# Performance work log

Hardware: AMD Instinct MI355X
Metric: run time of the kernel (lower is better)

## Reference

```python
import jax, jax.numpy as jnp
import numpy as np

B, A, NC, DIR, LMAX, MAXZ, NORB = 8, 64, 128, 4, 2, 10, 14
NF = NC * DIR * (2 * LMAX + 1)   # 2560
O2 = NORB * NORB                 # 196
AO = A * NORB                    # 896
LOG2 = float(np.log(2.0))

def ssp(v):  # spk shifted softplus
    return jax.nn.softplus(v) - LOG2

def setup_inputs():
    key = jax.random.key(0)
    ks = jax.random.split(key, 12)
    Z = jax.random.randint(ks[0], (B, A), 1, MAXZ)
    idx = np.arange(A)
    nbh_np = np.stack([np.delete(idx, i) for i in range(A)], 0)  # [A, A-1]: all atoms except self
    nbh = jnp.asarray(np.broadcast_to(nbh_np[None], (B, A, A - 1)).copy(), dtype=jnp.int32)
    x = jax.random.normal(ks[1], (B, A, NC), jnp.float32)
    Vijkl = jax.random.normal(ks[2], (B, A, A - 1, NF), jnp.float32) * 0.1
    sc = 1.0 / np.sqrt(NF)
    W_off = jax.random.normal(ks[3], (NF, O2), jnp.float32) * sc
    b_off = jnp.zeros((O2,), jnp.float32)
    W_on = jax.random.normal(ks[4], (NF, O2), jnp.float32) * sc
    b_on = jnp.zeros((O2,), jnp.float32)
    W_ovoff = jax.random.normal(ks[5], (NF, O2), jnp.float32) * sc
    b_ovoff = jnp.zeros((O2,), jnp.float32)
    ov_emb = jax.random.normal(ks[6], (MAXZ, O2), jnp.float32) * 0.1  # trainable overlap onsite embedding
    orb_energies = jax.random.normal(ks[7], (MAXZ, NORB), jnp.float32)  # h0 energies
    s0_energies = jnp.ones((MAXZ, NORB), jnp.float32)                   # s0 init = ones
    W1 = jax.random.normal(ks[8], (NC, NC // 2), jnp.float32) / np.sqrt(NC)
    b1 = jnp.zeros((NC // 2,), jnp.float32)
    W2 = jax.random.normal(ks[9], (NC // 2, 1), jnp.float32) / np.sqrt(NC // 2)
    b2 = jnp.zeros((1,), jnp.float32)
    return {"Z": Z, "nbh": nbh, "x": x, "Vijkl": Vijkl,
            "W_off": W_off, "b_off": b_off, "W_on": W_on, "b_on": b_on,
            "W_ovoff": W_ovoff, "b_ovoff": b_ovoff, "ov_emb": ov_emb,
            "orb_energies": orb_energies, "s0_energies": s0_energies,
            "W1": W1, "b1": b1, "W2": W2, "b2": b2}

def reference(Z, nbh, x, Vijkl, W_off, b_off, W_on, b_on, W_ovoff, b_ovoff,
              ov_emb, orb_energies, s0_energies, W1, b1, W2, b2):
    # permutation that reorders neighbor slots (plus appended zero/self slot) into atom order
    ar = jnp.broadcast_to(jnp.arange(A, dtype=nbh.dtype)[None, :, None], (B, A, 1))
    sort_idx = jnp.argsort(jnp.concatenate([nbh, ar], axis=2), axis=2)  # [B,A,A]
    eyeA = jnp.eye(A, dtype=Vijkl.dtype)
    eyeAO = jnp.eye(AO, dtype=Vijkl.dtype)

    def assemble(off, on):
        # off: [B,A,A-1,O2] pair blocks; on: [B,A,O2] onsite blocks
        offz = jnp.concatenate([off, jnp.zeros((B, A, 1, O2), off.dtype)], axis=2)  # zero self block at slot A-1
        offg = jnp.take_along_axis(offz, sort_idx[..., None], axis=2)               # [B,A,A,O2]
        M = offg + eyeA[None, :, :, None] * on[:, :, None, :]
        M = M.reshape(B, A, A, NORB, NORB).transpose(0, 1, 3, 2, 4).reshape(B, AO, AO)
        return 0.5 * (M + M.transpose(0, 2, 1))

    # Hamiltonian: offsite Dense + onsite Dense mean-aggregated over pairs
    H_off = Vijkl @ W_off + b_off                       # [B,A,A-1,O2]
    H_on = jnp.mean(Vijkl @ W_on + b_on, axis=2)        # [B,A,O2]
    H = assemble(H_off, H_on)
    # h0 single-atom diagonal (orb mask is all-active -> full diagonal)
    H = H + eyeAO[None] * orb_energies[Z].reshape(B, 1, AO)

    # Overlap: offsite Dense + onsite embedding lookup
    S_off = Vijkl @ W_ovoff + b_ovoff
    S_on = ov_emb[Z]                                    # [B,A,O2]
    S = assemble(S_off, S_on)
    S = S + eyeAO[None] * s0_energies[Z].reshape(B, 1, AO)

    # energy head: Dense->ssp->Dense->ScaleShift(0,1), sum over atoms
    Ei = ssp(x @ W1 + b1) @ W2 + b2                     # [B,A,1]
    E = jnp.sum(Ei, axis=1)                             # [B,1]
    return H, S, E
```

## Files before the change

kernel.cpp:

```cpp
#include <hip/hip_runtime.h>

#define B_      8
#define A_      64
#define NPAIR   63
#define NC_     128
#define NF_     2560
#define O2_     196
#define NORB_   14
#define AO_     896
#define NCOLS   588
#define CSTRIDE 640
#define KSTEPS  80
#define BM      128
#define BN      640

typedef short bf16x8 __attribute__((ext_vector_type(8)));
typedef float f32x4  __attribute__((ext_vector_type(4)));

__device__ __forceinline__ unsigned f2bf(float f) {
    unsigned u = __builtin_bit_cast(unsigned, f);
    return (u + 0x7fffu + ((u >> 16) & 1u)) >> 16;
}

__global__ void prep_w(const float* __restrict__ W_off, const float* __restrict__ W_ovoff,
                       const float* __restrict__ W_on, unsigned short* __restrict__ Bws) {
    __shared__ float wt[32 * BN];
    const int ks = blockIdx.x, t = threadIdx.x;
    for (int e = t; e < 32 * BN; e += 256) {
        int kl = e / BN, c = e - kl * BN;
        int kg = ks * 32 + kl;
        float v = 0.f;
        if (c < O2_)          v = W_off  [(size_t)kg * O2_ + c];
        else if (c < 2 * O2_) v = W_ovoff[(size_t)kg * O2_ + (c - O2_)];
        else if (c < 3 * O2_) v = W_on   [(size_t)kg * O2_ + (c - 2 * O2_)];
        wt[kl * BN + c] = v;
    }
    __syncthreads();
    char* out = (char*)(Bws + (size_t)ks * (BN * 32));
    for (int e = t; e < BN * 4; e += 256) {
        int n = e >> 2, sg = e & 3;
        uint4 w;
        w.x = f2bf(wt[(sg * 8 + 0) * BN + n]) | (f2bf(wt[(sg * 8 + 1) * BN + n]) << 16);
        w.y = f2bf(wt[(sg * 8 + 2) * BN + n]) | (f2bf(wt[(sg * 8 + 3) * BN + n]) << 16);
        w.z = f2bf(wt[(sg * 8 + 4) * BN + n]) | (f2bf(wt[(sg * 8 + 5) * BN + n]) << 16);
        w.w = f2bf(wt[(sg * 8 + 6) * BN + n]) | (f2bf(wt[(sg * 8 + 7) * BN + n]) << 16);
        unsigned byte = ((unsigned)(n * 64 + sg * 16)) ^ ((unsigned)(n & 7) << 4);
        *(uint4*)(out + byte) = w;
    }
}

__global__ __launch_bounds__(1024, 4)
void gemm_off(const float* __restrict__ V, const unsigned short* __restrict__ Bws,
              const float* __restrict__ b_off, const float* __restrict__ b_ovoff,
              const float* __restrict__ b_on, float* __restrict__ HSoff) {
    __shared__ alignas(16) unsigned short Alds[2][BM * 32];
    __shared__ alignas(16) unsigned short Blds[2][BN * 32];

    const int tid  = threadIdx.x;
    const int mt   = blockIdx.x;
    const int lane = tid & 63;
    const int wv   = tid >> 6;
    const int wm   = wv >> 2, wn = wv & 3;
    const int wvu  = __builtin_amdgcn_readfirstlane(wv);

    const int arow = tid >> 3, aseg = tid & 7;
    const float* aptr = V + (size_t)(mt * BM + arow) * NF_ + aseg * 4;

    f32x4 acc[2][10];
#pragma unroll
    for (int mf = 0; mf < 2; ++mf)
#pragma unroll
        for (int nf = 0; nf < 10; ++nf)
            acc[mf][nf] = (f32x4){0.f, 0.f, 0.f, 0.f};

    float4 pv;

    auto issueB = [&](int bf, int ks) {
        const unsigned short* src0 = Bws + (size_t)ks * (BN * 32) + lane * 8;
        unsigned short* dst0 = &Blds[bf][0];
        {
            __builtin_amdgcn_global_load_lds(
                (const __attribute__((address_space(1))) void*)(src0 + wvu * 512),
                (__attribute__((address_space(3))) void*)(dst0 + wvu * 512), 16, 0, 0);
        }
        {
            __builtin_amdgcn_global_load_lds(
                (const __attribute__((address_space(1))) void*)(src0 + (wvu + 16) * 512),
                (__attribute__((address_space(3))) void*)(dst0 + (wvu + 16) * 512), 16, 0, 0);
        }
        if (wvu < 8) {
            __builtin_amdgcn_global_load_lds(
                (const __attribute__((address_space(1))) void*)(src0 + (wvu + 32) * 512),
                (__attribute__((address_space(3))) void*)(dst0 + (wvu + 32) * 512), 16, 0, 0);
        }
    };
    auto loadA = [&](int ks) {
        pv = *(const float4*)(aptr + ks * 32);
    };
    auto writeA = [&](int bf) {
        uint2 w;
        w.x = f2bf(pv.x) | (f2bf(pv.y) << 16);
        w.y = f2bf(pv.z) | (f2bf(pv.w) << 16);
        unsigned byte = ((unsigned)(arow * 64 + aseg * 8)) ^ ((unsigned)(arow & 7) << 4);
        *(uint2*)((char*)&Alds[bf][0] + byte) = w;
    };
    auto compute = [&](int bf) {
        const int r0 = wm * 32 + (lane & 15);
        const int r1 = r0 + 16;
        const unsigned kb = (unsigned)(lane >> 4) * 16;
        const unsigned ab0 = ((unsigned)(r0 * 64) + kb) ^ ((unsigned)(r0 & 7) << 4);
        const unsigned ab1 = ((unsigned)(r1 * 64) + kb) ^ ((unsigned)(r1 & 7) << 4);
        bf16x8 af0 = *(const bf16x8*)((const char*)&Alds[bf][0] + ab0);
        bf16x8 af1 = *(const bf16x8*)((const char*)&Alds[bf][0] + ab1);
        const int nbase = wn * 160 + (lane & 15);
        const char* Bb = (const char*)&Blds[bf][0];
        bf16x8 bfr[2];
        {
            const int n0 = nbase;
            const unsigned b0 = ((unsigned)(n0 * 64) + kb) ^ ((unsigned)(n0 & 7) << 4);
            bfr[0] = *(const bf16x8*)(Bb + b0);
        }
#pragma unroll
        for (int nf = 0; nf < 10; ++nf) {
            if (nf < 9) {
                const int nn = nbase + (nf + 1) * 16;
                const unsigned bb = ((unsigned)(nn * 64) + kb) ^ ((unsigned)(nn & 7) << 4);
                bfr[(nf + 1) & 1] = *(const bf16x8*)(Bb + bb);
            }
            acc[0][nf] = __builtin_amdgcn_mfma_f32_16x16x32_bf16(af0, bfr[nf & 1], acc[0][nf], 0, 0, 0);
            acc[1][nf] = __builtin_amdgcn_mfma_f32_16x16x32_bf16(af1, bfr[nf & 1], acc[1][nf], 0, 0, 0);
        }
    };

    issueB(0, 0); loadA(0); writeA(0);
    __syncthreads();

    for (int ks = 0; ks < KSTEPS; ++ks) {
        const int cur = ks & 1, nxt = cur ^ 1;
        if (ks + 1 < KSTEPS) { issueB(nxt, ks + 1); loadA(ks + 1); }
        compute(cur);
        if (ks + 1 < KSTEPS) writeA(nxt);
        __syncthreads();
    }

    const int c16 = lane & 15, rg = lane >> 4;
#pragma unroll
    for (int nf = 0; nf < 10; ++nf) {
        int C = wn * 160 + nf * 16 + c16;
        if (C >= NCOLS) continue;
        float bias = (C < O2_) ? b_off[C] : (C < 2 * O2_) ? b_ovoff[C - O2_] : b_on[C - 2 * O2_];
#pragma unroll
        for (int mf = 0; mf < 2; ++mf) {
            int R = mt * BM + wm * 32 + mf * 16 + rg * 4;
            float* o = HSoff + (size_t)R * CSTRIDE + C;
            o[0]           = acc[mf][nf][0] + bias;
            o[CSTRIDE]     = acc[mf][nf][1] + bias;
            o[2 * CSTRIDE] = acc[mf][nf][2] + bias;
            o[3 * CSTRIDE] = acc[mf][nf][3] + bias;
        }
    }
}

__global__ void hon_reduce(const float* __restrict__ HSoff, float* __restrict__ Hon) {
    const int g = blockIdx.x;
    const int t = threadIdx.x;
    if (t >= O2_) return;
    const float* p0 = HSoff + (size_t)g * NPAIR * CSTRIDE + 2 * O2_ + t;
    const float* p1 = p0 + (size_t)21 * CSTRIDE;
    const float* p2 = p0 + (size_t)42 * CSTRIDE;
    float a0 = 0.f, a1 = 0.f, a2 = 0.f;
#pragma unroll 3
    for (int j = 0; j < 21; ++j) {
        a0 += p0[0]; a1 += p1[0]; a2 += p2[0];
        p0 += CSTRIDE; p1 += CSTRIDE; p2 += CSTRIDE;
    }
    Hon[(size_t)g * O2_ + t] = (a0 + a1 + a2) * (1.f / (float)NPAIR);
}

__global__ __launch_bounds__(256)
void assemble_k(const float* __restrict__ HSoff, const float* __restrict__ Hon,
                const int* __restrict__ Z, const float* __restrict__ ov_emb,
                const float* __restrict__ orbE, const float* __restrict__ s0E,
                float* __restrict__ H, float* __restrict__ S) {
    __shared__ float Ai[NPAIR * 197];
    __shared__ float Bj[2][16 * 200];
    __shared__ float Dg[O2_];
    __shared__ float Dd[NORB_];

    const int bid = blockIdx.x;
    const int h = bid & 1, i = (bid >> 1) & 63, b = bid >> 7;
    const int t = threadIdx.x;
    const int g = b * A_ + i;
    const int z = Z[g];
    float* out = (h ? S : H) + (size_t)b * AO_ * AO_;

    const float* abase = HSoff + (size_t)g * NPAIR * CSTRIDE + h * O2_;
    for (int u = t; u < NPAIR * O2_; u += 256) {
        int jj = u / O2_, e = u - jj * O2_;
        Ai[jj * 197 + e] = abase[(size_t)jj * CSTRIDE + e];
    }
    if (t < O2_)   Dg[t] = h ? ov_emb[(size_t)z * O2_ + t]   : Hon[(size_t)g * O2_ + t];
    if (t < NORB_) Dd[t] = h ? s0E[(size_t)z * NORB_ + t]    : orbE[(size_t)z * NORB_ + t];

    auto stageB = [&](int buf, int jc) {
        for (int u = t; u < 16 * O2_; u += 256) {
            int jl = u / O2_, e = u - jl * O2_;
            int j = jc * 16 + jl;
            if (j != i) {
                int idx = (i < j) ? i : i - 1;
                Bj[buf][jl * 200 + e] =
                    HSoff[((size_t)(b * A_ + j) * NPAIR + idx) * CSTRIDE + h * O2_ + e];
            }
        }
    };
    stageB(0, 0);
    __syncthreads();

    const int tj = t / NORB_, tq = t - tj * NORB_;
    for (int jc = 0; jc < 4; ++jc) {
        if (jc < 3) stageB((jc + 1) & 1, jc + 1);
        if (t < 224) {
            const int j = jc * 16 + tj;
            const int cur = jc & 1;
#pragma unroll
            for (int p = 0; p < NORB_; ++p) {
                float v;
                if (j == i) {
                    v = 0.5f * (Dg[p * NORB_ + tq] + Dg[tq * NORB_ + p]);
                    if (p == tq) v += Dd[p];
                } else {
                    int jj = (j < i) ? j : j - 1;
                    v = 0.5f * (Ai[jj * 197 + p * NORB_ + tq] + Bj[cur][tj * 200 + tq * NORB_ + p]);
                }
                out[(size_t)(i * NORB_ + p) * AO_ + jc * 224 + t] = v;
            }
        }
        __syncthreads();
    }
}

__global__ void energy_k(const float* __restrict__ x, const float* __restrict__ W1,
                         const float* __restrict__ b1, const float* __restrict__ W2,
                         const float* __restrict__ b2, float* __restrict__ E) {
    __shared__ float partial[8];
    const int b = blockIdx.x;
    const int lane = threadIdx.x & 63;
    const int w = threadIdx.x >> 6;
    float esum = 0.f;
    for (int aa = 0; aa < 8; ++aa) {
        const int a = w * 8 + aa;
        const float* xr = x + (size_t)(b * A_ + a) * NC_;
        float hj = b1[lane];
        for (int k = 0; k < NC_; ++k) hj = fmaf(xr[k], W1[k * 64 + lane], hj);
        float sp = fmaxf(hj, 0.f) + log1pf(expf(-fabsf(hj))) - 0.69314718055994531f;
        float v = sp * W2[lane];
        for (int off = 32; off; off >>= 1) v += __shfl_down(v, off);
        if (lane == 0) esum += v + b2[0];
    }
    if (lane == 0) partial[w] = esum;
    __syncthreads();
    if (threadIdx.x == 0) {
        float e = 0.f;
        for (int k = 0; k < 8; ++k) e += partial[k];
        E[b] = e;
    }
}

extern "C" void kernel_launch(void* const* d_in, const int* in_sizes, int n_in,
                              void* d_out, int out_size, void* d_ws, size_t ws_size,
                              hipStream_t stream) {
    const int*   Z       = (const int*)  d_in[0];
    const float* x       = (const float*)d_in[2];
    const float* V       = (const float*)d_in[3];
    const float* W_off   = (const float*)d_in[4];
    const float* b_off   = (const float*)d_in[5];
    const float* W_on    = (const float*)d_in[6];
    const float* b_on    = (const float*)d_in[7];
    const float* W_ovoff = (const float*)d_in[8];
    const float* b_ovoff = (const float*)d_in[9];
    const float* ov_emb  = (const float*)d_in[10];
    const float* orbE    = (const float*)d_in[11];
    const float* s0E     = (const float*)d_in[12];
    const float* W1      = (const float*)d_in[13];
    const float* b1      = (const float*)d_in[14];
    const float* W2      = (const float*)d_in[15];
    const float* b2      = (const float*)d_in[16];

    float* H = (float*)d_out;
    float* S = H + (size_t)B_ * AO_ * AO_;
    float* E = S + (size_t)B_ * AO_ * AO_;

    char* ws = (char*)d_ws;
    unsigned short* Bws = (unsigned short*)ws;
    float* HSoff = (float*)(ws + (size_t)4  * 1024 * 1024);
    float* Hon   = (float*)(ws + (size_t)88 * 1024 * 1024);

    prep_w    <<<KSTEPS, 256,  0, stream>>>(W_off, W_ovoff, W_on, Bws);
    gemm_off  <<<252,    1024, 0, stream>>>(V, Bws, b_off, b_ovoff, b_on, HSoff);
    hon_reduce<<<512,    256,  0, stream>>>(HSoff, Hon);
    assemble_k<<<1024,   256,  0, stream>>>(HSoff, Hon, Z, ov_emb, orbE, s0E, H, S);
    energy_k  <<<8,      512,  0, stream>>>(x, W1, b1, W2, b2, E);
}
```

Measured before the change: 308.8 us.

## Load B fragments directly from global into registers, drop B LDS staging

The GEMM no longer stages the bf16 weight tile through LDS. Each wave reads its B fragments straight from global/L2 into registers, with a software prefetch of the next k-step. Blocks shrink to 512 threads and each wave handles 64 rows (4 M fragments), so every B fragment feeds four MFMAs, and the A tile is written with 16-byte stores. The aim is to cut LDS traffic and barrier cost, at the price of many more global loads of B and much higher register pressure, which can limit occupancy.

Measured after the change: 307.5 us. No clear change (-0.4%).

```diff
diff --git a/kernel.cpp b/kernel.cpp
--- a/kernel.cpp
+++ b/kernel.cpp
@@ -13,6 +13,7 @@
 #define KSTEPS  80
 #define BM      128
 #define BN      640
+#define BSTEP_BYTES 40960
 
 typedef short bf16x8 __attribute__((ext_vector_type(8)));
 typedef float f32x4  __attribute__((ext_vector_type(4)));
@@ -36,7 +37,7 @@
         wt[kl * BN + c] = v;
     }
     __syncthreads();
-    char* out = (char*)(Bws + (size_t)ks * (BN * 32));
+    unsigned short* out = Bws + (size_t)ks * (BN * 32);
     for (int e = t; e < BN * 4; e += 256) {
         int n = e >> 2, sg = e & 3;
         uint4 w;
@@ -44,103 +45,97 @@
         w.y = f2bf(wt[(sg * 8 + 2) * BN + n]) | (f2bf(wt[(sg * 8 + 3) * BN + n]) << 16);
         w.z = f2bf(wt[(sg * 8 + 4) * BN + n]) | (f2bf(wt[(sg * 8 + 5) * BN + n]) << 16);
         w.w = f2bf(wt[(sg * 8 + 6) * BN + n]) | (f2bf(wt[(sg * 8 + 7) * BN + n]) << 16);
-        unsigned byte = ((unsigned)(n * 64 + sg * 16)) ^ ((unsigned)(n & 7) << 4);
-        *(uint4*)(out + byte) = w;
-    }
-}
-
-__global__ __launch_bounds__(1024, 4)
+        *(uint4*)(out + (size_t)n * 32 + sg * 8) = w;
+    }
+}
+
+__global__ __launch_bounds__(512, 2)
 void gemm_off(const float* __restrict__ V, const unsigned short* __restrict__ Bws,
               const float* __restrict__ b_off, const float* __restrict__ b_ovoff,
               const float* __restrict__ b_on, float* __restrict__ HSoff) {
     __shared__ alignas(16) unsigned short Alds[2][BM * 32];
-    __shared__ alignas(16) unsigned short Blds[2][BN * 32];
 
     const int tid  = threadIdx.x;
     const int mt   = blockIdx.x;
     const int lane = tid & 63;
     const int wv   = tid >> 6;
     const int wm   = wv >> 2, wn = wv & 3;
-    const int wvu  = __builtin_amdgcn_readfirstlane(wv);
-
-    const int arow = tid >> 3, aseg = tid & 7;
-    const float* aptr = V + (size_t)(mt * BM + arow) * NF_ + aseg * 4;
-
-    f32x4 acc[2][10];
-#pragma unroll
-    for (int mf = 0; mf < 2; ++mf)
+
+    const int arow = tid >> 2, aseg = tid & 3;
+    const float* aptr = V + (size_t)(mt * BM + arow) * NF_ + aseg * 8;
+
+    const char* bp = (const char*)Bws + (size_t)(wn * 160 + (lane & 15)) * 64 + (lane >> 4) * 16;
+#define BFRAG(t_, nf_) (*(const bf16x8*)(bp + (size_t)(t_) * BSTEP_BYTES + (nf_) * 1024))
+
+    f32x4 acc[4][10];
+#pragma unroll
+    for (int mf = 0; mf < 4; ++mf)
 #pragma unroll
         for (int nf = 0; nf < 10; ++nf)
             acc[mf][nf] = (f32x4){0.f, 0.f, 0.f, 0.f};
 
-    float4 pv;
-
-    auto issueB = [&](int bf, int ks) {
-        const unsigned short* src0 = Bws + (size_t)ks * (BN * 32) + lane * 8;
-        unsigned short* dst0 = &Blds[bf][0];
-        {
-            __builtin_amdgcn_global_load_lds(
-                (const __attribute__((address_space(1))) void*)(src0 + wvu * 512),
-                (__attribute__((address_space(3))) void*)(dst0 + wvu * 512), 16, 0, 0);
-        }
-        {
-            __builtin_amdgcn_global_load_lds(
-                (const __attribute__((address_space(1))) void*)(src0 + (wvu + 16) * 512),
-                (__attribute__((address_space(3))) void*)(dst0 + (wvu + 16) * 512), 16, 0, 0);
-        }
-        if (wvu < 8) {
-            __builtin_amdgcn_global_load_lds(
-                (const __attribute__((address_space(1))) void*)(src0 + (wvu + 32) * 512),
-                (__attribute__((address_space(3))) void*)(dst0 + (wvu + 32) * 512), 16, 0, 0);
-        }
-    };
+    float4 pv0, pv1;
     auto loadA = [&](int ks) {
-        pv = *(const float4*)(aptr + ks * 32);
+        const float* s = aptr + ks * 32;
+        pv0 = ((const float4*)s)[0];
+        pv1 = ((const float4*)s)[1];
     };
     auto writeA = [&](int bf) {
-        uint2 w;
-        w.x = f2bf(pv.x) | (f2bf(pv.y) << 16);
-        w.y = f2bf(pv.z) | (f2bf(pv.w) << 16);
-        unsigned byte = ((unsigned)(arow * 64 + aseg * 8)) ^ ((unsigned)(arow & 7) << 4);
-        *(uint2*)((char*)&Alds[bf][0] + byte) = w;
+        uint4 w;
+        w.x = f2bf(pv0.x) | (f2bf(pv0.y) << 16);
+        w.y = f2bf(pv0.z) | (f2bf(pv0.w) << 16);
+        w.z = f2bf(pv1.x) | (f2bf(pv1.y) << 16);
+        w.w = f2bf(pv1.z) | (f2bf(pv1.w) << 16);
+        unsigned byte = ((unsigned)(arow * 64 + aseg * 16)) ^ ((unsigned)(arow & 7) << 4);
+        *(uint4*)((char*)&Alds[bf][0] + byte) = w;
     };
-    auto compute = [&](int bf) {
-        const int r0 = wm * 32 + (lane & 15);
-        const int r1 = r0 + 16;
-        const unsigned kb = (unsigned)(lane >> 4) * 16;
-        const unsigned ab0 = ((unsigned)(r0 * 64) + kb) ^ ((unsigned)(r0 & 7) << 4);
-        const unsigned ab1 = ((unsigned)(r1 * 64) + kb) ^ ((unsigned)(r1 & 7) << 4);
-        bf16x8 af0 = *(const bf16x8*)((const char*)&Alds[bf][0] + ab0);
-        bf16x8 af1 = *(const bf16x8*)((const char*)&Alds[bf][0] + ab1);
-        const int nbase = wn * 160 + (lane & 15);
-        const char* Bb = (const char*)&Blds[bf][0];
-        bf16x8 bfr[2];
-        {
-            const int n0 = nbase;
-            const unsigned b0 = ((unsigned)(n0 * 64) + kb) ^ ((unsigned)(n0 & 7) << 4);
-            bfr[0] = *(const bf16x8*)(Bb + b0);
+
+    const int ar = wm * 64 + (lane & 15);
+    const unsigned kb = (unsigned)(lane >> 4) * 16;
+
+#define ARD(mf_) (*(const bf16x8*)((const char*)Ab + ((((unsigned)((ar + (mf_) * 16) * 64) + kb)) ^ ((unsigned)(ar & 7) << 4))))
+
+#define MFMA4(bv_, nf_) {                                                                  \
+    acc[0][nf_] = __builtin_amdgcn_mfma_f32_16x16x32_bf16(af0, bv_, acc[0][nf_], 0, 0, 0); \
+    acc[1][nf_] = __builtin_amdgcn_mfma_f32_16x16x32_bf16(af1, bv_, acc[1][nf_], 0, 0, 0); \
+    acc[2][nf_] = __builtin_amdgcn_mfma_f32_16x16x32_bf16(af2, bv_, acc[2][nf_], 0, 0, 0); \
+    acc[3][nf_] = __builtin_amdgcn_mfma_f32_16x16x32_bf16(af3, bv_, acc[3][nf_], 0, 0, 0); }
+
+    bf16x8 bq0, bq1, bq2, bq3, bq4;
+
+    loadA(0);
+    writeA(0);
+    bq0 = BFRAG(0, 0); bq1 = BFRAG(0, 1); bq2 = BFRAG(0, 2); bq3 = BFRAG(0, 3); bq4 = BFRAG(0, 4);
+    loadA(1);
+    asm volatile("s_waitcnt lgkmcnt(0)" ::: "memory");
+    __builtin_amdgcn_s_barrier();
+    __builtin_amdgcn_sched_barrier(0);
+
+    int cur = 0;
+    for (int t = 0; t < KSTEPS; ++t) {
+        const unsigned short* Ab = &Alds[cur][0];
+        bf16x8 af0 = ARD(0), af1 = ARD(1), af2 = ARD(2), af3 = ARD(3);
+
+        MFMA4(bq0, 0); bq0 = BFRAG(t, 5);
+        MFMA4(bq1, 1); bq1 = BFRAG(t, 6);
+        MFMA4(bq2, 2); bq2 = BFRAG(t, 7);
+        MFMA4(bq3, 3); bq3 = BFRAG(t, 8);
+        MFMA4(bq4, 4); bq4 = BFRAG(t, 9);
+        MFMA4(bq0, 5); bq0 = BFRAG(t + 1, 0);
+        MFMA4(bq1, 6); bq1 = BFRAG(t + 1, 1);
+        MFMA4(bq2, 7); bq2 = BFRAG(t + 1, 2);
+        MFMA4(bq3, 8); bq3 = BFRAG(t + 1, 3);
+        MFMA4(bq4, 9); bq4 = BFRAG(t + 1, 4);
+
+        if (t < KSTEPS - 1) {
+            writeA(cur ^ 1);
+            int ks2 = t + 2 < KSTEPS ? t + 2 : KSTEPS - 1;
+            loadA(ks2);
+            asm volatile("s_waitcnt lgkmcnt(0)" ::: "memory");
+            __builtin_amdgcn_s_barrier();
+            __builtin_amdgcn_sched_barrier(0);
         }
-#pragma unroll
-        for (int nf = 0; nf < 10; ++nf) {
-            if (nf < 9) {
-                const int nn = nbase + (nf + 1) * 16;
-                const unsigned bb = ((unsigned)(nn * 64) + kb) ^ ((unsigned)(nn & 7) << 4);
-                bfr[(nf + 1) & 1] = *(const bf16x8*)(Bb + bb);
-            }
-            acc[0][nf] = __builtin_amdgcn_mfma_f32_16x16x32_bf16(af0, bfr[nf & 1], acc[0][nf], 0, 0, 0);
-            acc[1][nf] = __builtin_amdgcn_mfma_f32_16x16x32_bf16(af1, bfr[nf & 1], acc[1][nf], 0, 0, 0);
-        }
-    };
-
-    issueB(0, 0); loadA(0); writeA(0);
-    __syncthreads();
-
-    for (int ks = 0; ks < KSTEPS; ++ks) {
-        const int cur = ks & 1, nxt = cur ^ 1;
-        if (ks + 1 < KSTEPS) { issueB(nxt, ks + 1); loadA(ks + 1); }
-        compute(cur);
-        if (ks + 1 < KSTEPS) writeA(nxt);
-        __syncthreads();
+        cur ^= 1;
     }
 
     const int c16 = lane & 15, rg = lane >> 4;
@@ -150,8 +145,8 @@
         if (C >= NCOLS) continue;
         float bias = (C < O2_) ? b_off[C] : (C < 2 * O2_) ? b_ovoff[C - O2_] : b_on[C - 2 * O2_];
 #pragma unroll
-        for (int mf = 0; mf < 2; ++mf) {
-            int R = mt * BM + wm * 32 + mf * 16 + rg * 4;
+        for (int mf = 0; mf < 4; ++mf) {
+            int R = mt * BM + wm * 64 + mf * 16 + rg * 4;
             float* o = HSoff + (size_t)R * CSTRIDE + C;
             o[0]           = acc[mf][nf][0] + bias;
             o[CSTRIDE]     = acc[mf][nf][1] + bias;
@@ -159,6 +154,9 @@
             o[3 * CSTRIDE] = acc[mf][nf][3] + bias;
         }
     }
+#undef BFRAG
+#undef ARD
+#undef MFMA4
 }
 
 __global__ void hon_reduce(const float* __restrict__ HSoff, float* __restrict__ Hon) {
@@ -295,9 +293,9 @@
     float* HSoff = (float*)(ws + (size_t)4  * 1024 * 1024);
     float* Hon   = (float*)(ws + (size_t)88 * 1024 * 1024);
 
-    prep_w    <<<KSTEPS, 256,  0, stream>>>(W_off, W_ovoff, W_on, Bws);
-    gemm_off  <<<252,    1024, 0, stream>>>(V, Bws, b_off, b_ovoff, b_on, HSoff);
-    hon_reduce<<<512,    256,  0, stream>>>(HSoff, Hon);
-    assemble_k<<<1024,   256,  0, stream>>>(HSoff, Hon, Z, ov_emb, orbE, s0E, H, S);
-    energy_k  <<<8,      512,  0, stream>>>(x, W1, b1, W2, b2, E);
-}
+    prep_w    <<<KSTEPS, 256, 0, stream>>>(W_off, W_ovoff, W_on, Bws);
+    gemm_off  <<<252,    512, 0, stream>>>(V, Bws, b_off, b_ovoff, b_on, HSoff);
+    hon_reduce<<<512,    256, 0, stream>>>(HSoff, Hon);
+    assemble_k<<<1024,   256, 0, stream>>>(HSoff, Hon, Z, ov_emb, orbE, s0E, H, S);
+    energy_k  <<<8,      512, 0, stream>>>(x, W1, b1, W2, b2, E);
+}
```
